# Optimization experiments

Measured on AMD Instinct MI355X. Metric: run time of the kernel, lower is better.

## Reference

```python
import jax, jax.numpy as jnp
import numpy as np

B, T, D, H = 1024, 512, 256, 256  # batch, seq_len, input_dim, hidden_dim


def setup_inputs() -> dict:
    key = jax.random.key(0)
    ks = jax.random.split(key, 7)
    std = 1.0 / np.sqrt(H)  # matches GRUCell.reset_parameters uniform(-std, std)
    u = lambda k, shape: jax.random.uniform(k, shape, jnp.float32, -std, std)
    return {
        "x": jax.random.normal(ks[0], (B, T, D), jnp.float32),
        "Wx": u(ks[1], (3 * H, D)),   # x2h weight
        "bx": u(ks[2], (3 * H,)),     # x2h bias
        "Wh": u(ks[3], (3 * H, H)),   # h2h weight
        "bh": u(ks[4], (3 * H,)),     # h2h bias
        "Wa": u(ks[5], (H, 2 * H)),   # attention gate weight
        "ba": u(ks[6], (H,)),         # attention gate bias
    }


def reference(x, Wx, bx, Wh, bh, Wa, ba):
    # GRUModel: sequential scan of attention-gated GRUCell over seq dim.
    # Precompute all input projections in one big GEMM (time-independent).
    gx_all = jnp.einsum("btd,gd->btg", x, Wx) + bx  # [B, T, 3H]

    def step(h, gx):
        gh = h @ Wh.T + bh                     # [B, 3H]
        i_r, i_i, i_n = jnp.split(gx, 3, axis=-1)
        h_r, h_i, h_n = jnp.split(gh, 3, axis=-1)
        resetgate = jax.nn.sigmoid(i_r + h_r)
        att_in = jnp.concatenate([i_i, h_i], axis=-1)  # [B, 2H]
        inputgate = jax.nn.sigmoid(att_in @ Wa.T + ba)
        newgate = jnp.tanh(i_n + resetgate * h_n)
        hy = newgate + inputgate * (h - newgate)
        return hy, hy

    h0 = jnp.zeros((x.shape[0], Wh.shape[1]), x.dtype)
    _, outs = jax.lax.scan(step, h0, jnp.swapaxes(gx_all, 0, 1))  # [T, B, H]
    return jnp.swapaxes(outs, 0, 1)  # [B, T, H]
```

## Files before the change

kernel.cpp:

```cpp
#include <hip/hip_runtime.h>
#include <stdint.h>
#include <stddef.h>

#define Bsz 1024
#define Tsz 512
#define Dsz 256
#define Hsz 256
#define SLAB 24576

typedef __bf16 bf16;
typedef __attribute__((ext_vector_type(8))) __bf16 bf16x8;
typedef __attribute__((ext_vector_type(4))) float f32x4;

#define MFMA __builtin_amdgcn_mfma_f32_16x16x32_bf16

__device__ __forceinline__ float sigm(float x) {
  return __builtin_amdgcn_rcpf(1.f + exp2f(-1.4426950408889634f * x));
}
__device__ __forceinline__ float bflo(uint32_t v) {
  union { uint32_t u; float f; } c; c.u = v << 16; return c.f;
}
__device__ __forceinline__ float bfhi(uint32_t v) {
  union { uint32_t u; float f; } c; c.u = v & 0xffff0000u; return c.f;
}
__device__ __forceinline__ bf16x8 asb(uint4 u) {
  union { uint4 a; bf16x8 b; } c; c.a = u; return c.b;
}
#define PIN4(v) asm volatile("" : "+v"((v).x), "+v"((v).y), "+v"((v).z), "+v"((v).w))

__global__ __launch_bounds__(256) void k_repack(
    const float* __restrict__ Wx, const float* __restrict__ Wh,
    bf16* __restrict__ wxf, bf16* __restrict__ whf) {
  int g = blockIdx.x * 256 + threadIdx.x;
  int gg = g & 16383;
  int lr = gg & 15, lq = (gg >> 4) & 3, kp = (gg >> 6) & 7, tile = gg >> 9;
  int row = (tile < 16) ? (tile * 16 + lr) : (512 + (tile - 16) * 16 + lr);
  const float* s;
  bf16* d;
  if (g < 16384) { s = Wx + row * 256 + kp * 32 + lq * 8; d = wxf + gg * 8; }
  else           { s = Wh + row * 256 + kp * 32 + lq * 8; d = whf + gg * 8; }
  #pragma unroll
  for (int e = 0; e < 8; ++e) d[e] = (bf16)s[e];
}

__global__ __launch_bounds__(256) void k_wc(
    const float* __restrict__ Wa, const float* __restrict__ Wh,
    const float* __restrict__ Wx, const float* __restrict__ bh,
    const float* __restrict__ bx, const float* __restrict__ ba,
    bf16* __restrict__ wcf, bf16* __restrict__ wxf, float* __restrict__ c0) {
  __shared__ float red[256];
  int n = blockIdx.x, k = threadIdx.x;
  float accC = 0.f, accP = 0.f;
  for (int m = 0; m < 256; ++m) {
    accC += Wa[n * 512 + 256 + m] * Wh[(256 + m) * 256 + k];
    accP += Wa[n * 512 + m]       * Wx[(256 + m) * 256 + k];
  }
  int kp = k >> 5, lq = (k >> 3) & 3, e = k & 7;
  int ti = n >> 4, lr = n & 15;
  wcf[(ti * 8 + kp) * 512 + lq * 128 + lr * 8 + e] = (bf16)accC;
  wxf[(((32 + ti) * 8) + kp) * 512 + lq * 128 + lr * 8 + e] = (bf16)accP;
  red[k] = Wa[n * 512 + 256 + k] * bh[256 + k] + Wa[n * 512 + k] * bx[256 + k];
  __syncthreads();
  for (int s = 128; s > 0; s >>= 1) {
    if (k < s) red[k] += red[k + s];
    __syncthreads();
  }
  if (k == 0) c0[n] = ba[n] + red[0];
}

__global__ __launch_bounds__(256) __attribute__((amdgpu_waves_per_eu(1, 1)))
void k_phase1(
    const float* __restrict__ x, const bf16* __restrict__ wxf,
    const float* __restrict__ bx, const float* __restrict__ bh,
    const float* __restrict__ c0, bf16* __restrict__ gx, int t0, int TP) {
  int tid = threadIdx.x;
  int w = tid >> 6, l = tid & 63, lr = l & 15, lq = l >> 4;
  int bg = blockIdx.x, b0 = bg << 4;
  int tl0 = blockIdx.y * TP;
  int loffE = lq * 128 + lr * 8;

  uint4 W[12][8];
  float bias[12];
  #pragma unroll
  for (int i = 0; i < 12; ++i) {
    int ft = w * 12 + i;
    #pragma unroll
    for (int kk = 0; kk < 8; ++kk) {
      W[i][kk] = *(const uint4*)(wxf + (size_t)(ft * 8 + kk) * 512 + loffE);
      PIN4(W[i][kk]);
    }
    int rgn = ft >> 4, r = (ft & 15) * 16 + lr;
    bias[i] = (rgn == 0) ? bx[r] + bh[r]
            : (rgn == 1) ? bx[512 + r]
            : c0[r];
  }
  const float* xbase = x + (size_t)(b0 + lr) * (Tsz * Dsz) + lq * 8;
  #pragma unroll 1
  for (int tt = 0; tt < TP; ++tt) {
    int tloc = tl0 + tt;
    const float* xp = xbase + (size_t)(t0 + tloc) * Dsz;
    bf16x8 A[8];
    #pragma unroll
    for (int kk = 0; kk < 8; ++kk) {
      float4 f0 = *(const float4*)(xp + kk * 32);
      float4 f1 = *(const float4*)(xp + kk * 32 + 4);
      bf16x8 a;
      a[0] = (bf16)f0.x; a[1] = (bf16)f0.y; a[2] = (bf16)f0.z; a[3] = (bf16)f0.w;
      a[4] = (bf16)f1.x; a[5] = (bf16)f1.y; a[6] = (bf16)f1.z; a[7] = (bf16)f1.w;
      A[kk] = a;
    }
    char* sb = (char*)gx + ((size_t)tloc * 64 + bg) * SLAB;
    #pragma unroll
    for (int g = 0; g < 4; ++g) {
      f32x4 acc[3];
      #pragma unroll
      for (int i2 = 0; i2 < 3; ++i2)
        #pragma unroll
        for (int e = 0; e < 4; ++e) acc[i2][e] = bias[g * 3 + i2];
      #pragma unroll
      for (int kk = 0; kk < 8; ++kk)
        #pragma unroll
        for (int i2 = 0; i2 < 3; ++i2)
          acc[i2] = MFMA(A[kk], asb(W[g * 3 + i2][kk]), acc[i2], 0, 0, 0);
      #pragma unroll
      for (int i2 = 0; i2 < 3; ++i2) {
        int ft = w * 12 + g * 3 + i2;
        union { bf16 v[4]; uint2 u; } pk;
        #pragma unroll
        for (int j = 0; j < 4; ++j) pk.v[j] = (bf16)acc[i2][j];
        *(uint2*)(sb + (ft >> 4) * 8192 + (ft & 15) * 512 + loffE) = pk.u;
      }
    }
  }
}

__global__ __launch_bounds__(512) __attribute__((amdgpu_waves_per_eu(2, 2)))
void k_phase2(
    const bf16* __restrict__ gx, const bf16* __restrict__ whf,
    const bf16* __restrict__ wcf, const float* __restrict__ bh,
    float* __restrict__ out, float* __restrict__ hstate, int t0, int TC) {
  extern __shared__ char lds[];
  char* hb0 = lds + 131072;
  int tid = threadIdx.x;
  int w = tid >> 6, l = tid & 63, lr = l & 15, lq = l >> 4;
  int bg = blockIdx.x, b0 = bg << 4;
  int loffE = lq * 128 + lr * 8;

  #pragma unroll 4
  for (int it = 0; it < 16; ++it)
    *(uint4*)(lds + it * 8192 + tid * 16) =
        *(const uint4*)((const char*)wcf + it * 8192 + tid * 16);

  uint4 wR[2][8], wN[2][8];
  #pragma unroll
  for (int p = 0; p < 2; ++p)
    #pragma unroll
    for (int kk = 0; kk < 8; ++kk) {
      int ct = 2 * w + p;
      wR[p][kk] = *(const uint4*)(whf + (size_t)(ct * 8 + kk) * 512 + loffE);
      wN[p][kk] = *(const uint4*)(whf + (size_t)((16 + ct) * 8 + kk) * 512 + loffE);
      PIN4(wR[p][kk]); PIN4(wN[p][kk]);
    }
  float bN[2];
  bN[0] = bh[512 + (2 * w + 0) * 16 + lr];
  bN[1] = bh[512 + (2 * w + 1) * 16 + lr];

  float h[2][4];
  #pragma unroll
  for (int p = 0; p < 2; ++p) {
    int col = (2 * w + p) * 16 + lr;
    #pragma unroll
    for (int j = 0; j < 4; ++j)
      h[p][j] = (t0 == 0) ? 0.f : hstate[(size_t)(b0 + 4 * lq + j) * Hsz + col];
    int cb = ((col >> 5) << 10) + (((col >> 3) & 3) << 8) + (lq << 6) + ((col & 7) << 1);
    char* hw = hb0 + cb;
    #pragma unroll
    for (int j = 0; j < 4; ++j) *(bf16*)(hw + j * 16) = (bf16)h[p][j];
  }
  __syncthreads();

  const char* gxb = (const char*)gx + (size_t)bg * SLAB;
  const size_t tstride = (size_t)64 * SLAB;
  uint2 gR[2], gN[2], gA[2];
  #pragma unroll
  for (int p = 0; p < 2; ++p) {
    int toff = (2 * w + p) * 512 + loffE;
    gR[p] = *(const uint2*)(gxb + toff);
    gN[p] = *(const uint2*)(gxb + 8192 + toff);
    gA[p] = *(const uint2*)(gxb + 16384 + toff);
  }

  #pragma unroll 1
  for (int t = 0; t < TC; ++t) {
    int cur = t & 1, nxt = cur ^ 1;
    const char* hc = hb0 + cur * 8192 + lq * 256 + lr * 16;
    char* hn = hb0 + nxt * 8192;
    bf16x8 Ah[8];
    #pragma unroll
    for (int kk = 0; kk < 8; ++kk) Ah[kk] = *(const bf16x8*)(hc + kk * 1024);
    bool pf = (t + 1 < TC);
    const char* sl = gxb + (size_t)(t + 1) * tstride;
    f32x4 aR[2], aN[2], aA[2];
    #pragma unroll
    for (int p = 0; p < 2; ++p)
      #pragma unroll
      for (int e = 0; e < 4; ++e) { aR[p][e] = 0.f; aN[p][e] = bN[p]; aA[p][e] = 0.f; }
    #pragma unroll
    for (int kk = 0; kk < 8; ++kk) {
      aR[0] = MFMA(Ah[kk], asb(wR[0][kk]), aR[0], 0, 0, 0);
      aR[1] = MFMA(Ah[kk], asb(wR[1][kk]), aR[1], 0, 0, 0);
      aN[0] = MFMA(Ah[kk], asb(wN[0][kk]), aN[0], 0, 0, 0);
      aN[1] = MFMA(Ah[kk], asb(wN[1][kk]), aN[1], 0, 0, 0);
      bf16x8 wc0 = *(const bf16x8*)(lds + (size_t)((2 * w + 0) * 8 + kk) * 1024 + lq * 256 + lr * 16);
      aA[0] = MFMA(Ah[kk], wc0, aA[0], 0, 0, 0);
      bf16x8 wc1 = *(const bf16x8*)(lds + (size_t)((2 * w + 1) * 8 + kk) * 1024 + lq * 256 + lr * 16);
      aA[1] = MFMA(Ah[kk], wc1, aA[1], 0, 0, 0);
    }
    #pragma unroll
    for (int p = 0; p < 2; ++p) {
      float irj[4] = { bflo(gR[p].x), bfhi(gR[p].x), bflo(gR[p].y), bfhi(gR[p].y) };
      float inj[4] = { bflo(gN[p].x), bfhi(gN[p].x), bflo(gN[p].y), bfhi(gN[p].y) };
      float aij[4] = { bflo(gA[p].x), bfhi(gA[p].x), bflo(gA[p].y), bfhi(gA[p].y) };
      int col = (2 * w + p) * 16 + lr;
      #pragma unroll
      for (int j = 0; j < 4; ++j) {
        float rg = sigm(irj[j] + aR[p][j]);
        float xx = inj[j] + rg * aN[p][j];
        xx = fminf(fmaxf(xx, -15.f), 15.f);
        float e2 = exp2f(-2.885390081777927f * xx);
        float ng = (1.f - e2) * __builtin_amdgcn_rcpf(1.f + e2);
        float ig = sigm(aij[j] + aA[p][j]);
        h[p][j] = ng + ig * (h[p][j] - ng);
      }
      int cb = ((col >> 5) << 10) + (((col >> 3) & 3) << 8) + (lq << 6) + ((col & 7) << 1);
      char* hw = hn + cb;
      #pragma unroll
      for (int j = 0; j < 4; ++j) *(bf16*)(hw + j * 16) = (bf16)h[p][j];
      #pragma unroll
      for (int j = 0; j < 4; ++j)
        out[(size_t)(b0 + 4 * lq + j) * (Tsz * Hsz) + (size_t)(t0 + t) * Hsz + col] = h[p][j];
      if (pf) {
        int toff = (2 * w + p) * 512 + loffE;
        gR[p] = *(const uint2*)(sl + toff);
        gN[p] = *(const uint2*)(sl + 8192 + toff);
        gA[p] = *(const uint2*)(sl + 16384 + toff);
      }
    }
    asm volatile("s_waitcnt lgkmcnt(0)" ::: "memory");
    __builtin_amdgcn_s_barrier();
    __builtin_amdgcn_sched_barrier(0);
  }
  #pragma unroll
  for (int p = 0; p < 2; ++p) {
    int col = (2 * w + p) * 16 + lr;
    #pragma unroll
    for (int j = 0; j < 4; ++j)
      hstate[(size_t)(b0 + 4 * lq + j) * Hsz + col] = h[p][j];
  }
}

extern "C" void kernel_launch(void* const* d_in, const int* in_sizes, int n_in,
                              void* d_out, int out_size, void* d_ws, size_t ws_size,
                              hipStream_t stream) {
  (void)in_sizes; (void)n_in; (void)out_size;
  const float* x  = (const float*)d_in[0];
  const float* Wx = (const float*)d_in[1];
  const float* bx = (const float*)d_in[2];
  const float* Wh = (const float*)d_in[3];
  const float* bh = (const float*)d_in[4];
  const float* Wa = (const float*)d_in[5];
  const float* ba = (const float*)d_in[6];
  float* out = (float*)d_out;
  char* ws = (char*)d_ws;

  bf16* wxf = (bf16*)ws;
  bf16* whf = (bf16*)(ws + 393216);
  bf16* wcf = (bf16*)(ws + 655360);
  float* c0 = (float*)(ws + 786432);
  float* hstate = (float*)(ws + 1048576);
  bf16* gxbuf = (bf16*)(ws + 2097152);

  size_t avail = (ws_size > 2097152) ? ws_size - 2097152 : 0;
  size_t per_t = (size_t)64 * SLAB;
  long tcl = (long)(avail / per_t);
  int TC = (tcl > Tsz) ? Tsz : (int)tcl;
  TC &= ~63;
  if (TC < 64) TC = 64;

  (void)hipFuncSetAttribute((const void*)k_phase2,
                            hipFuncAttributeMaxDynamicSharedMemorySize, 147456);

  k_repack<<<dim3(128), dim3(256), 0, stream>>>(Wx, Wh, wxf, whf);
  k_wc<<<dim3(256), dim3(256), 0, stream>>>(Wa, Wh, Wx, bh, bx, ba, wcf, wxf, c0);
  for (int t0 = 0; t0 < Tsz; t0 += TC) {
    int tc = Tsz - t0; if (tc > TC) tc = TC;
    int TP = tc / 4;
    k_phase1<<<dim3(64, 4), dim3(256), 0, stream>>>(x, wxf, bx, bh, c0, gxbuf, t0, TP);
    k_phase2<<<dim3(64), dim3(512), 147456, stream>>>(gxbuf, whf, wcf, bh, out, hstate, t0, tc);
  }
}
```

Measured before the change: 2.048 ms.

## Split phase1 weights across 8 waves, pin weights in AGPRs, software-pipeline x loads

The input-projection kernel now uses 512 threads, so each wave keeps 6 weight tiles instead of 12. The register-pinned weights in both phases are forced into accumulator registers (AGPRs) instead of VGPRs. Biases move to shared memory, and the x loads are double-buffered so they overlap with the MFMAs. The launch grid now adapts TP to the chunk size. The aim is more waves and better overlap of latency, at the cost of possible AGPR-to-VGPR copies feeding the MFMA operands.

After: 2.314 ms. +13.0%, slower.

```diff
diff --git a/kernel.cpp b/kernel.cpp
--- a/kernel.cpp
+++ b/kernel.cpp
@@ -26,7 +26,7 @@
 __device__ __forceinline__ bf16x8 asb(uint4 u) {
   union { uint4 a; bf16x8 b; } c; c.a = u; return c.b;
 }
-#define PIN4(v) asm volatile("" : "+v"((v).x), "+v"((v).y), "+v"((v).z), "+v"((v).w))
+#define PIN4A(v) asm volatile("" : "+a"((v).x), "+a"((v).y), "+a"((v).z), "+a"((v).w))
 
 __global__ __launch_bounds__(256) void k_repack(
     const float* __restrict__ Wx, const float* __restrict__ Wh,
@@ -68,68 +68,72 @@
   if (k == 0) c0[n] = ba[n] + red[0];
 }
 
-__global__ __launch_bounds__(256) __attribute__((amdgpu_waves_per_eu(1, 1)))
+__global__ __launch_bounds__(512) __attribute__((amdgpu_waves_per_eu(2, 2)))
 void k_phase1(
     const float* __restrict__ x, const bf16* __restrict__ wxf,
     const float* __restrict__ bx, const float* __restrict__ bh,
     const float* __restrict__ c0, bf16* __restrict__ gx, int t0, int TP) {
+  __shared__ float biasL[768];
   int tid = threadIdx.x;
   int w = tid >> 6, l = tid & 63, lr = l & 15, lq = l >> 4;
   int bg = blockIdx.x, b0 = bg << 4;
   int tl0 = blockIdx.y * TP;
   int loffE = lq * 128 + lr * 8;
-
-  uint4 W[12][8];
-  float bias[12];
-  #pragma unroll
-  for (int i = 0; i < 12; ++i) {
-    int ft = w * 12 + i;
+  for (int i = tid; i < 768; i += 512) {
+    float v;
+    if (i < 256)      v = bx[i] + bh[i];
+    else if (i < 512) v = bx[256 + i];
+    else              v = c0[i - 512];
+    biasL[i] = v;
+  }
+  uint4 W[6][8];
+  #pragma unroll
+  for (int i = 0; i < 6; ++i) {
+    int ft = w * 6 + i;
     #pragma unroll
     for (int kk = 0; kk < 8; ++kk) {
       W[i][kk] = *(const uint4*)(wxf + (size_t)(ft * 8 + kk) * 512 + loffE);
-      PIN4(W[i][kk]);
-    }
-    int rgn = ft >> 4, r = (ft & 15) * 16 + lr;
-    bias[i] = (rgn == 0) ? bx[r] + bh[r]
-            : (rgn == 1) ? bx[512 + r]
-            : c0[r];
-  }
-  const float* xbase = x + (size_t)(b0 + lr) * (Tsz * Dsz) + lq * 8;
+      PIN4A(W[i][kk]);
+    }
+  }
+  __syncthreads();
+  const float* xrow = x + (size_t)(b0 + lr) * (Tsz * Dsz) + lq * 8;
   #pragma unroll 1
   for (int tt = 0; tt < TP; ++tt) {
     int tloc = tl0 + tt;
-    const float* xp = xbase + (size_t)(t0 + tloc) * Dsz;
-    bf16x8 A[8];
+    const float* xp = xrow + (size_t)(t0 + tloc) * Dsz;
+    float4 lA[2], lB[2];
+    lA[0] = *(const float4*)(xp);
+    lB[0] = *(const float4*)(xp + 4);
+    f32x4 acc[6];
+    #pragma unroll
+    for (int i = 0; i < 6; ++i) {
+      float bv = biasL[(w * 6 + i) * 16 + lr];
+      #pragma unroll
+      for (int e = 0; e < 4; ++e) acc[i][e] = bv;
+    }
     #pragma unroll
     for (int kk = 0; kk < 8; ++kk) {
-      float4 f0 = *(const float4*)(xp + kk * 32);
-      float4 f1 = *(const float4*)(xp + kk * 32 + 4);
+      if (kk < 7) {
+        lA[(kk + 1) & 1] = *(const float4*)(xp + (kk + 1) * 32);
+        lB[(kk + 1) & 1] = *(const float4*)(xp + (kk + 1) * 32 + 4);
+      }
+      float4 f0 = lA[kk & 1], f1 = lB[kk & 1];
       bf16x8 a;
       a[0] = (bf16)f0.x; a[1] = (bf16)f0.y; a[2] = (bf16)f0.z; a[3] = (bf16)f0.w;
       a[4] = (bf16)f1.x; a[5] = (bf16)f1.y; a[6] = (bf16)f1.z; a[7] = (bf16)f1.w;
-      A[kk] = a;
+      #pragma unroll
+      for (int i = 0; i < 6; ++i)
+        acc[i] = MFMA(a, asb(W[i][kk]), acc[i], 0, 0, 0);
     }
     char* sb = (char*)gx + ((size_t)tloc * 64 + bg) * SLAB;
     #pragma unroll
-    for (int g = 0; g < 4; ++g) {
-      f32x4 acc[3];
-      #pragma unroll
-      for (int i2 = 0; i2 < 3; ++i2)
-        #pragma unroll
-        for (int e = 0; e < 4; ++e) acc[i2][e] = bias[g * 3 + i2];
-      #pragma unroll
-      for (int kk = 0; kk < 8; ++kk)
-        #pragma unroll
-        for (int i2 = 0; i2 < 3; ++i2)
-          acc[i2] = MFMA(A[kk], asb(W[g * 3 + i2][kk]), acc[i2], 0, 0, 0);
-      #pragma unroll
-      for (int i2 = 0; i2 < 3; ++i2) {
-        int ft = w * 12 + g * 3 + i2;
-        union { bf16 v[4]; uint2 u; } pk;
-        #pragma unroll
-        for (int j = 0; j < 4; ++j) pk.v[j] = (bf16)acc[i2][j];
-        *(uint2*)(sb + (ft >> 4) * 8192 + (ft & 15) * 512 + loffE) = pk.u;
-      }
+    for (int i = 0; i < 6; ++i) {
+      int ft = w * 6 + i;
+      union { bf16 v[4]; uint2 u; } pk;
+      #pragma unroll
+      for (int j = 0; j < 4; ++j) pk.v[j] = (bf16)acc[i][j];
+      *(uint2*)(sb + (ft >> 4) * 8192 + (ft & 15) * 512 + loffE) = pk.u;
     }
   }
 }
@@ -159,7 +163,7 @@
       int ct = 2 * w + p;
       wR[p][kk] = *(const uint4*)(whf + (size_t)(ct * 8 + kk) * 512 + loffE);
       wN[p][kk] = *(const uint4*)(whf + (size_t)((16 + ct) * 8 + kk) * 512 + loffE);
-      PIN4(wR[p][kk]); PIN4(wN[p][kk]);
+      PIN4A(wR[p][kk]); PIN4A(wN[p][kk]);
     }
   float bN[2];
   bN[0] = bh[512 + (2 * w + 0) * 16 + lr];
@@ -294,8 +298,8 @@
   k_wc<<<dim3(256), dim3(256), 0, stream>>>(Wa, Wh, Wx, bh, bx, ba, wcf, wxf, c0);
   for (int t0 = 0; t0 < Tsz; t0 += TC) {
     int tc = Tsz - t0; if (tc > TC) tc = TC;
-    int TP = tc / 4;
-    k_phase1<<<dim3(64, 4), dim3(256), 0, stream>>>(x, wxf, bx, bh, c0, gxbuf, t0, TP);
+    int TP = (tc % 128 == 0) ? 128 : 64;
+    k_phase1<<<dim3(64, tc / TP), dim3(512), 0, stream>>>(x, wxf, bx, bh, c0, gxbuf, t0, TP);
     k_phase2<<<dim3(64), dim3(512), 147456, stream>>>(gxbuf, whf, wcf, bh, out, hstate, t0, tc);
   }
 }
```
